# Kernel tuning notes

Hardware: AMD Instinct MI355X
Metric: run time of the kernel (lower is better)

Reference implementation:

```python
import jax, jax.numpy as jnp
import numpy as np

NUM_HEADS = 8
EPS = 1e-12  # matches torch F.normalize default eps


def setup_inputs() -> dict:
    key = jax.random.key(0)
    k1, k2 = jax.random.split(key)
    x = jax.random.normal(k1, (8, 384, 128, 128), dtype=jnp.float32)
    # 1x1 conv weight [out=3*dim, in=dim]
    w_qkv = jax.random.normal(k2, (1152, 384), dtype=jnp.float32) * (1.0 / np.sqrt(384))
    return {"x": x, "w_qkv": w_qkv}


def _l2norm(t):
    # torch F.normalize(dim=-1): x / max(||x||2, eps)
    n = jnp.sqrt(jnp.sum(t * t, axis=-1, keepdims=True))
    return t / jnp.maximum(n, EPS)


def reference(x, w_qkv):
    B, C, H, W = x.shape
    hw = H * W
    head_c = C // NUM_HEADS
    # 1x1 conv == channel matmul
    qkv = jnp.einsum('bchw,oc->bohw', x, w_qkv)  # [B, 3C, H, W]
    q, k, v = jnp.split(qkv, 3, axis=1)
    def rs(t):
        return t.reshape(B, NUM_HEADS, head_c, hw)
    q, k, v = rs(q), rs(k), rs(v)
    q = _l2norm(q)
    k = _l2norm(k)
    scale = jnp.sqrt(jnp.float32(hw))
    attn = jnp.einsum('bhcn,bhdn->bhcd', q, k) / scale  # small CxC per head
    attn = jax.nn.softmax(attn, axis=-1)
    out = jnp.einsum('bhcd,bhdn->bhcn', attn, v)
    return out.reshape(B, C, H, W)
```

## Files before the change

kernel.cpp:

```cpp
#include <hip/hip_runtime.h>

typedef short short8 __attribute__((ext_vector_type(8)));
typedef __bf16 bf16x8 __attribute__((ext_vector_type(8)));
typedef float f32x4 __attribute__((ext_vector_type(4)));
typedef int i32x4 __attribute__((ext_vector_type(4)));

typedef const __attribute__((address_space(1))) void* gas_p;
typedef __attribute__((address_space(3))) void* las_p;

static __device__ __forceinline__ unsigned short f2bf(float f) {
  unsigned u = __builtin_bit_cast(unsigned, f);
  u += 0x7fffu + ((u >> 16) & 1u);
  return (unsigned short)(u >> 16);
}
static __device__ __forceinline__ float bf2f(unsigned short h) {
  unsigned u = ((unsigned)h) << 16;
  return __builtin_bit_cast(float, u);
}

#define MFMA16(a, b, c) __builtin_amdgcn_mfma_f32_16x16x32_bf16( \
    __builtin_bit_cast(bf16x8, a), __builtin_bit_cast(bf16x8, b), (c), 0, 0, 0)

__global__ __launch_bounds__(64) void k0_wfrag(const float* __restrict__ w,
                                               unsigned short* __restrict__ wfrag) {
  int bx = blockIdx.x;
  int m16 = bx / 12, kb = bx % 12;
  int lane = threadIdx.x;
  int i = lane & 15, g = lane >> 4;
  int o = m16 * 16 + i;
  int k = kb * 32 + g * 8;
  const float* src = w + (size_t)o * 384 + k;
  f32x4 f0 = *(const f32x4*)(src);
  f32x4 f1 = *(const f32x4*)(src + 4);
  short8 v;
#pragma unroll
  for (int j = 0; j < 4; ++j) { v[j] = (short)f2bf(f0[j]); v[4 + j] = (short)f2bf(f1[j]); }
  *(short8*)(wfrag + ((size_t)(m16 * 12 + kb) * 64 + lane) * 8) = v;
}

__global__ __launch_bounds__(256) void kx_transpose(const float* __restrict__ x,
                                                    unsigned short* __restrict__ xt,
                                                    int bbase) {
  __shared__ unsigned T[64 * 32];
  int n0 = blockIdx.x * 64, c0 = blockIdx.y * 64;
  int bl = blockIdx.z;
  int bg = bbase + bl;
  int t = threadIdx.x;
  int cl2 = t >> 6, nl = t & 63;
  const float* xb = x + ((size_t)bg * 384 + c0) * 16384 + n0 + nl;
#pragma unroll
  for (int u = 0; u < 8; ++u) {
    int cb = cl2 * 2 + u * 8;
    float f0 = xb[(size_t)cb * 16384];
    float f1 = xb[(size_t)(cb + 1) * 16384];
    unsigned p = (unsigned)f2bf(f0) | ((unsigned)f2bf(f1) << 16);
    int cp = cb >> 1;
    T[nl * 32 + (cp ^ (nl & 31))] = p;
  }
  __syncthreads();
  int nl2 = t >> 2, cg = t & 3;
  unsigned vals[8];
#pragma unroll
  for (int j = 0; j < 8; ++j)
    vals[j] = T[nl2 * 32 + ((cg * 8 + j) ^ (nl2 & 31))];
  unsigned short* dst = xt + ((size_t)bl * 16384 + n0 + nl2) * 384 + c0 + cg * 16;
  *(i32x4*)(dst)     = (i32x4){(int)vals[0], (int)vals[1], (int)vals[2], (int)vals[3]};
  *(i32x4*)(dst + 8) = (i32x4){(int)vals[4], (int)vals[5], (int)vals[6], (int)vals[7]};
}

__global__ __launch_bounds__(256, 4) void k1_qkv(const unsigned short* __restrict__ xt,
                                                 const unsigned short* __restrict__ wfrag,
                                                 unsigned short* __restrict__ qkv,
                                                 float* __restrict__ norms2,
                                                 int bbase, int nb) {
  __shared__ union {
    unsigned short Bt[2][128 * 32];
    unsigned short Cl[128 * 136];
  } sm;

  int flat = blockIdx.x;
  int b_l = flat % nb;
  int rem = flat / nb;
  int m = rem % 9, ntile = rem / 9;
  int o0 = m * 128, n0 = ntile * 128;
  int bg = bbase + b_l;
  int t = threadIdx.x;
  int wave = t >> 6, lane = t & 63;
  int i = lane & 15, g = lane >> 4;
  int mh = wave >> 1, nh = wave & 1;

  int r = t >> 2, blk = t & 3;
  int srcblk = blk ^ (r & 3);
  const unsigned short* xrow =
      xt + ((size_t)b_l * 16384 + n0 + r) * 384 + srcblk * 8;

  const unsigned short* wbase = wfrag + ((size_t)(m * 8 + mh * 4) * 12 * 64 + lane) * 8;

#define STAGE(buf, kb)                                                          \
  do {                                                                          \
    const unsigned short* s0 = xrow + (kb) * 32;                                \
    unsigned short* d0 = &sm.Bt[0][0] + (buf) * 4096 + t * 8;                   \
    __builtin_amdgcn_global_load_lds((gas_p)s0, (las_p)d0, 16, 0, 0);           \
    __builtin_amdgcn_global_load_lds((gas_p)(s0 + (size_t)64 * 384),            \
                                     (las_p)(d0 + 2048), 16, 0, 0);             \
  } while (0)

  f32x4 acc[4][4];
#pragma unroll
  for (int a = 0; a < 4; ++a)
#pragma unroll
    for (int c = 0; c < 4; ++c) acc[a][c] = (f32x4){0.f, 0.f, 0.f, 0.f};

  short8 aF[4];
#pragma unroll
  for (int mt = 0; mt < 4; ++mt)
    aF[mt] = *(const short8*)(wbase + (size_t)(mt * 12) * 512);
  STAGE(0, 0);

#pragma unroll
  for (int kb = 0; kb < 12; ++kb) {
    __syncthreads();
    short8 aFn[4];
    if (kb < 11) {
      STAGE((kb + 1) & 1, kb + 1);
#pragma unroll
      for (int mt = 0; mt < 4; ++mt)
        aFn[mt] =
            *(const short8*)(wbase + (size_t)(mt * 12 + kb + 1) * 512);
    }
    const unsigned short* bb = &sm.Bt[kb & 1][0];
    int swz = (g ^ (i & 3)) * 8;
#pragma unroll
    for (int nt = 0; nt < 4; ++nt) {
      short8 bF = *(const short8*)(bb + (nh * 64 + nt * 16 + i) * 32 + swz);
#pragma unroll
      for (int mt = 0; mt < 4; ++mt) acc[mt][nt] = MFMA16(aF[mt], bF, acc[mt][nt]);
    }
    if (kb < 11) {
#pragma unroll
      for (int mt = 0; mt < 4; ++mt) aF[mt] = aFn[mt];
    }
  }
#undef STAGE

  __syncthreads();

#pragma unroll
  for (int mt = 0; mt < 4; ++mt)
#pragma unroll
    for (int nt = 0; nt < 4; ++nt)
#pragma unroll
      for (int rr = 0; rr < 4; ++rr)
        sm.Cl[(mh * 64 + mt * 16 + 4 * g + rr) * 136 + nh * 64 + nt * 16 + i] =
            f2bf(acc[mt][nt][rr]);
  __syncthreads();

  size_t obase = ((size_t)bg * 1152 + o0) * 16384 + n0;
  int srow = t >> 4, scol = (t & 15) * 8;
#pragma unroll
  for (int u = 0; u < 8; ++u) {
    int row = u * 16 + srow;
    short8 vv = *(const short8*)&sm.Cl[row * 136 + scol];
    *(short8*)(qkv + obase + (size_t)row * 16384 + scol) = vv;
  }

  if (o0 < 768) {
    int row = t >> 1, half = t & 1;
    const unsigned short* p = &sm.Cl[row * 136 + half * 64];
    float s = 0.f;
#pragma unroll
    for (int u = 0; u < 8; ++u) {
      short8 vv = *(const short8*)(p + u * 8);
#pragma unroll
      for (int e = 0; e < 8; ++e) {
        float f = bf2f((unsigned short)vv[e]);
        s += f * f;
      }
    }
    s += __shfl_xor(s, 1, 64);
    if (half == 0) atomicAdd(&norms2[bg * 768 + o0 + row], s);
  }
}

__global__ __launch_bounds__(256) void k2_gram(const unsigned short* __restrict__ qkv,
                                               float* __restrict__ Gpart) {
  __shared__ union {
    unsigned short Bt[2][96 * 128];
    float Gl[48 * 48];
  } sm;
  int bh = blockIdx.x >> 3, chunk = blockIdx.x & 7;
  int b = bh >> 3, hi = bh & 7;
  int t = threadIdx.x, wave = t >> 6, lane = t & 63;
  int i = lane & 15, g = lane >> 4;

  const unsigned short* qrow = qkv + ((size_t)b * 1152 + hi * 48) * 16384;
  const unsigned short* krow = qrow + (size_t)384 * 16384;
  int P = chunk * 2048;

  int srow = t >> 4;
  int sblk = (t & 15) ^ (srow & 7);

#define STAGE2(buf, tt)                                                         \
  do {                                                                          \
    int p0 = P + (tt) * 128 + sblk * 8;                                         \
    unsigned short* d0 = &sm.Bt[buf][0] + t * 8;                                \
    _Pragma("unroll")                                                           \
    for (int e = 0; e < 3; ++e) {                                               \
      __builtin_amdgcn_global_load_lds(                                         \
          (gas_p)(qrow + (size_t)(e * 16 + srow) * 16384 + p0),                 \
          (las_p)(d0 + e * 2048), 16, 0, 0);                                    \
      __builtin_amdgcn_global_load_lds(                                         \
          (gas_p)(krow + (size_t)(e * 16 + srow) * 16384 + p0),                 \
          (las_p)(d0 + (e + 3) * 2048), 16, 0, 0);                              \
    }                                                                           \
  } while (0)

  f32x4 acc[3][3];
#pragma unroll
  for (int a = 0; a < 3; ++a)
#pragma unroll
    for (int c = 0; c < 3; ++c) acc[a][c] = (f32x4){0.f, 0.f, 0.f, 0.f};

  STAGE2(0, 0);
  int ksg = wave * 4 + g;
  for (int tt = 0; tt < 16; ++tt) {
    __syncthreads();
    if (tt < 15) STAGE2((tt + 1) & 1, tt + 1);
    const unsigned short* bb = &sm.Bt[tt & 1][0];
    int d = (ksg ^ (i & 7)) * 8;
    short8 aF[3], bF[3];
#pragma unroll
    for (int mt = 0; mt < 3; ++mt)
      aF[mt] = *(const short8*)(bb + (mt * 16 + i) * 128 + d);
#pragma unroll
    for (int nt = 0; nt < 3; ++nt)
      bF[nt] = *(const short8*)(bb + (48 + nt * 16 + i) * 128 + d);
#pragma unroll
    for (int mt = 0; mt < 3; ++mt)
#pragma unroll
      for (int nt = 0; nt < 3; ++nt) acc[mt][nt] = MFMA16(aF[mt], bF[nt], acc[mt][nt]);
  }
#undef STAGE2

  __syncthreads();
  for (int u = t; u < 2304; u += 256) sm.Gl[u] = 0.f;
  __syncthreads();
#pragma unroll
  for (int mt = 0; mt < 3; ++mt)
#pragma unroll
    for (int nt = 0; nt < 3; ++nt)
#pragma unroll
      for (int rr = 0; rr < 4; ++rr)
        atomicAdd(&sm.Gl[(mt * 16 + 4 * g + rr) * 48 + nt * 16 + i],
                  acc[mt][nt][rr]);
  __syncthreads();
  float* Gg = Gpart + (size_t)(bh * 8 + chunk) * 2304;
  for (int u = t; u < 2304; u += 256) Gg[u] = sm.Gl[u];
}

__global__ __launch_bounds__(256) void k2b_softmax(const float* __restrict__ Gpart,
                                                   const float* __restrict__ norms2,
                                                   float* __restrict__ attn) {
  __shared__ float Gl[2304];
  int bh = blockIdx.x;
  int b = bh >> 3, hi = bh & 7;
  int t = threadIdx.x;
  const float* base = Gpart + (size_t)bh * 8 * 2304;
  for (int u = t; u < 2304; u += 256) {
    float s = 0.f;
#pragma unroll
    for (int ch = 0; ch < 8; ++ch) s += base[(size_t)ch * 2304 + u];
    Gl[u] = s;
  }
  __syncthreads();
  if (t >= 48) return;
  int c = t;
  const float* nq = norms2 + b * 768 + hi * 48;
  const float* nk = nq + 384;
  float dq = fmaxf(sqrtf(nq[c]), 1e-12f);
  float l[48];
  float m = -1e30f;
#pragma unroll
  for (int d = 0; d < 48; ++d) {
    float dk = fmaxf(sqrtf(nk[d]), 1e-12f);
    l[d] = Gl[c * 48 + d] / (dq * dk * 128.0f);
    m = fmaxf(m, l[d]);
  }
  float s = 0.f;
#pragma unroll
  for (int d = 0; d < 48; ++d) {
    l[d] = expf(l[d] - m);
    s += l[d];
  }
  float inv = 1.0f / s;
  float* A = attn + (size_t)bh * 2304 + c * 48;
#pragma unroll
  for (int d = 0; d < 48; ++d) A[d] = l[d] * inv;
}

__global__ __launch_bounds__(256) void k3_out(const unsigned short* __restrict__ qkv,
                                              const float* __restrict__ attn,
                                              float* __restrict__ out) {
  __shared__ unsigned short Vt[256 * 72];
  int nchunk = blockIdx.x, bh = blockIdx.y;
  int b = bh >> 3, hi = bh & 7;
  int n0 = nchunk * 256;
  int t = threadIdx.x, wave = t >> 6, lane = t & 63;
  int i = lane & 15, g = lane >> 4;

  const unsigned short* vbase = qkv + ((size_t)b * 1152 + 768 + hi * 48) * 16384 + n0 + t;
  unsigned short* vr = &Vt[t * 72];
#pragma unroll
  for (int dp = 0; dp < 24; ++dp) {
    unsigned a0 = vbase[(size_t)(2 * dp) * 16384];
    unsigned a1 = vbase[(size_t)(2 * dp + 1) * 16384];
    *(unsigned*)(vr + 2 * dp) = a0 | (a1 << 16);
  }
  *(i32x4*)(vr + 48) = (i32x4){0, 0, 0, 0};
  *(i32x4*)(vr + 56) = (i32x4){0, 0, 0, 0};

  const float* Ab = attn + (size_t)bh * 2304;
  short8 aF[3][2];
#pragma unroll
  for (int mt = 0; mt < 3; ++mt) {
    int row = mt * 16 + i;
    f32x4 f0 = *(const f32x4*)(Ab + row * 48 + 8 * g);
    f32x4 f1 = *(const f32x4*)(Ab + row * 48 + 8 * g + 4);
    short8 a0;
#pragma unroll
    for (int j = 0; j < 4; ++j) { a0[j] = (short)f2bf(f0[j]); a0[4 + j] = (short)f2bf(f1[j]); }
    aF[mt][0] = a0;
    short8 a1v = (short8){0, 0, 0, 0, 0, 0, 0, 0};
    if (g < 2) {
      f32x4 h0 = *(const f32x4*)(Ab + row * 48 + 32 + 8 * g);
      f32x4 h1 = *(const f32x4*)(Ab + row * 48 + 32 + 8 * g + 4);
#pragma unroll
      for (int j = 0; j < 4; ++j) { a1v[j] = (short)f2bf(h0[j]); a1v[4 + j] = (short)f2bf(h1[j]); }
    }
    aF[mt][1] = a1v;
  }
  __syncthreads();

  f32x4 acc[3][4];
#pragma unroll
  for (int a = 0; a < 3; ++a)
#pragma unroll
    for (int c = 0; c < 4; ++c) acc[a][c] = (f32x4){0.f, 0.f, 0.f, 0.f};

  int nb = wave * 64;
#pragma unroll
  for (int nt = 0; nt < 4; ++nt) {
    const unsigned short* vp = &Vt[(size_t)(nb + nt * 16 + i) * 72 + 8 * g];
    short8 b0 = *(const short8*)vp;
    short8 b1 = *(const short8*)(vp + 32);
#pragma unroll
    for (int mt = 0; mt < 3; ++mt) {
      acc[mt][nt] = MFMA16(aF[mt][0], b0, acc[mt][nt]);
      acc[mt][nt] = MFMA16(aF[mt][1], b1, acc[mt][nt]);
    }
  }

  float* ob = out + ((size_t)b * 384 + hi * 48) * 16384 + n0 + nb;
#pragma unroll
  for (int mt = 0; mt < 3; ++mt)
#pragma unroll
    for (int nt = 0; nt < 4; ++nt)
#pragma unroll
      for (int rr = 0; rr < 4; ++rr)
        ob[(size_t)(mt * 16 + 4 * g + rr) * 16384 + nt * 16 + i] = acc[mt][nt][rr];
}

extern "C" void kernel_launch(void* const* d_in, const int* in_sizes, int n_in,
                              void* d_out, int out_size, void* d_ws, size_t ws_size,
                              hipStream_t stream) {
  const float* x = (const float*)d_in[0];
  const float* w = (const float*)d_in[1];
  float* out = (float*)d_out;
  char* ws = (char*)d_ws;

  unsigned short* qkv   = (unsigned short*)(ws);
  unsigned short* wfrag = (unsigned short*)(ws + 301989888LL);
  float* norms2         = (float*)(ws + 302874624LL);
  float* attn           = (float*)(ws + 303489024LL);
  unsigned short* xtb   = (unsigned short*)(ws + 304078848LL);
  float* Gpart          = (float*)xtb;

  const size_t FULL_NEED = 304078848LL + 100663296LL;

  hipMemsetAsync(ws + 302874624LL, 0, 24576, stream);
  k0_wfrag<<<864, 64, 0, stream>>>(w, wfrag);

  if (ws_size >= FULL_NEED) {
    kx_transpose<<<dim3(256, 6, 8), 256, 0, stream>>>(x, xtb, 0);
    k1_qkv<<<9216, 256, 0, stream>>>(xtb, wfrag, qkv, norms2, 0, 8);
  } else {
    for (int b = 0; b < 8; ++b) {
      kx_transpose<<<dim3(256, 6, 1), 256, 0, stream>>>(x, xtb, b);
      k1_qkv<<<1152, 256, 0, stream>>>(xtb, wfrag, qkv, norms2, b, 1);
    }
  }

  k2_gram<<<512, 256, 0, stream>>>(qkv, Gpart);
  k2b_softmax<<<64, 256, 0, stream>>>(Gpart, norms2, attn);
  k3_out<<<dim3(64, 64), 256, 0, stream>>>(qkv, attn, out);
}
```

Baseline: 390.9 us.

## Give each wave a private N-slice in the QKV GEMM and drop block barriers

The QKV projection kernel now has each of the four waves compute all 128 output rows for its own 32-column slice, instead of a 2x2 wave grid. Each wave stages only its own activation rows into LDS and reads only those, so the per-iteration __syncthreads is replaced by explicit vmcnt waits. The aim is to remove block-wide barrier stalls and let waves run out of step with one another. In exchange, each wave now loads twice as many weight fragments from global memory and keeps twice as many weight registers live, so the occupancy hint drops from 4 to 3 blocks per CU.

Result: slower. 630.8 us (+61.4%).

```diff
diff --git a/kernel.cpp b/kernel.cpp
--- a/kernel.cpp
+++ b/kernel.cpp
@@ -68,13 +68,13 @@
   *(i32x4*)(dst + 8) = (i32x4){(int)vals[4], (int)vals[5], (int)vals[6], (int)vals[7]};
 }
 
-__global__ __launch_bounds__(256, 4) void k1_qkv(const unsigned short* __restrict__ xt,
+__global__ __launch_bounds__(256, 3) void k1_qkv(const unsigned short* __restrict__ xt,
                                                  const unsigned short* __restrict__ wfrag,
                                                  unsigned short* __restrict__ qkv,
                                                  float* __restrict__ norms2,
                                                  int bbase, int nb) {
   __shared__ union {
-    unsigned short Bt[2][128 * 32];
+    unsigned short Bt[2][4096];
     unsigned short Cl[128 * 136];
   } sm;
 
@@ -87,58 +87,62 @@
   int t = threadIdx.x;
   int wave = t >> 6, lane = t & 63;
   int i = lane & 15, g = lane >> 4;
-  int mh = wave >> 1, nh = wave & 1;
-
-  int r = t >> 2, blk = t & 3;
-  int srcblk = blk ^ (r & 3);
-  const unsigned short* xrow =
-      xt + ((size_t)b_l * 16384 + n0 + r) * 384 + srcblk * 8;
-
-  const unsigned short* wbase = wfrag + ((size_t)(m * 8 + mh * 4) * 12 * 64 + lane) * 8;
-
-#define STAGE(buf, kb)                                                          \
-  do {                                                                          \
-    const unsigned short* s0 = xrow + (kb) * 32;                                \
-    unsigned short* d0 = &sm.Bt[0][0] + (buf) * 4096 + t * 8;                   \
-    __builtin_amdgcn_global_load_lds((gas_p)s0, (las_p)d0, 16, 0, 0);           \
-    __builtin_amdgcn_global_load_lds((gas_p)(s0 + (size_t)64 * 384),            \
-                                     (las_p)(d0 + 2048), 16, 0, 0);             \
+
+  int rl = lane >> 2;
+  int blk = lane & 3;
+  int srcblk = blk ^ (rl & 3);
+  const unsigned short* xr0 =
+      xt + ((size_t)b_l * 16384 + n0 + wave * 32) * 384;
+
+  const unsigned short* wbase = wfrag + ((size_t)(m * 8) * 12 * 64 + lane) * 8;
+
+#define STAGE(buf, kb)                                                         \
+  do {                                                                         \
+    _Pragma("unroll")                                                          \
+    for (int e = 0; e < 2; ++e)                                                \
+      __builtin_amdgcn_global_load_lds(                                        \
+          (gas_p)(xr0 + (size_t)(e * 16 + rl) * 384 + (kb) * 32 + srcblk * 8), \
+          (las_p)(&sm.Bt[buf][wave * 1024 + e * 512 + lane * 8]), 16, 0, 0);   \
   } while (0)
 
-  f32x4 acc[4][4];
-#pragma unroll
-  for (int a = 0; a < 4; ++a)
-#pragma unroll
-    for (int c = 0; c < 4; ++c) acc[a][c] = (f32x4){0.f, 0.f, 0.f, 0.f};
-
-  short8 aF[4];
-#pragma unroll
-  for (int mt = 0; mt < 4; ++mt)
+  f32x4 acc[8][2];
+#pragma unroll
+  for (int a = 0; a < 8; ++a)
+#pragma unroll
+    for (int c = 0; c < 2; ++c) acc[a][c] = (f32x4){0.f, 0.f, 0.f, 0.f};
+
+  short8 aF[8];
+#pragma unroll
+  for (int mt = 0; mt < 8; ++mt)
     aF[mt] = *(const short8*)(wbase + (size_t)(mt * 12) * 512);
   STAGE(0, 0);
 
 #pragma unroll
   for (int kb = 0; kb < 12; ++kb) {
-    __syncthreads();
-    short8 aFn[4];
+    short8 aFn[8];
     if (kb < 11) {
       STAGE((kb + 1) & 1, kb + 1);
 #pragma unroll
-      for (int mt = 0; mt < 4; ++mt)
-        aFn[mt] =
-            *(const short8*)(wbase + (size_t)(mt * 12 + kb + 1) * 512);
-    }
-    const unsigned short* bb = &sm.Bt[kb & 1][0];
-    int swz = (g ^ (i & 3)) * 8;
-#pragma unroll
-    for (int nt = 0; nt < 4; ++nt) {
-      short8 bF = *(const short8*)(bb + (nh * 64 + nt * 16 + i) * 32 + swz);
-#pragma unroll
-      for (int mt = 0; mt < 4; ++mt) acc[mt][nt] = MFMA16(aF[mt], bF, acc[mt][nt]);
-    }
+      for (int mt = 0; mt < 8; ++mt)
+        aFn[mt] = *(const short8*)(wbase + (size_t)(mt * 12 + kb + 1) * 512);
+    }
+    __builtin_amdgcn_sched_barrier(0);
     if (kb < 11) {
-#pragma unroll
-      for (int mt = 0; mt < 4; ++mt) aF[mt] = aFn[mt];
+      asm volatile("s_waitcnt vmcnt(10)" ::: "memory");
+    } else {
+      asm volatile("s_waitcnt vmcnt(0)" ::: "memory");
+    }
+    __builtin_amdgcn_sched_barrier(0);
+    const unsigned short* bb = &sm.Bt[kb & 1][wave * 1024];
+#pragma unroll
+    for (int nt = 0; nt < 2; ++nt) {
+      short8 bF = *(const short8*)(bb + (nt * 16 + i) * 32 + (g ^ (i & 3)) * 8);
+#pragma unroll
+      for (int mt = 0; mt < 8; ++mt) acc[mt][nt] = MFMA16(aF[mt], bF, acc[mt][nt]);
+    }
+    if (kb < 11) {
+#pragma unroll
+      for (int mt = 0; mt < 8; ++mt) aF[mt] = aFn[mt];
     }
   }
 #undef STAGE
@@ -146,12 +150,12 @@
   __syncthreads();
 
 #pragma unroll
-  for (int mt = 0; mt < 4; ++mt)
-#pragma unroll
-    for (int nt = 0; nt < 4; ++nt)
+  for (int mt = 0; mt < 8; ++mt)
+#pragma unroll
+    for (int nt = 0; nt < 2; ++nt)
 #pragma unroll
       for (int rr = 0; rr < 4; ++rr)
-        sm.Cl[(mh * 64 + mt * 16 + 4 * g + rr) * 136 + nh * 64 + nt * 16 + i] =
+        sm.Cl[(mt * 16 + 4 * g + rr) * 136 + wave * 32 + nt * 16 + i] =
             f2bf(acc[mt][nt][rr]);
   __syncthreads();
 
```
